# Optimization experiments

Measured on AMD Instinct MI355X. Metric: run time of the kernel, lower is better.

The kernel has to match this reference:

```python
import jax, jax.numpy as jnp
import numpy as np

B, N, D = 16, 4096, 512   # batch, channels, d_model
R, K = 64, 128            # regions, channels per region


def setup_inputs() -> dict:
    key = jax.random.key(0)
    k1, k2, k3 = jax.random.split(key, 3)
    x = jax.random.normal(k1, (B, N, D), dtype=jnp.float32)
    region_indices = jax.random.randint(k2, (R, K), 0, N)
    W = jax.random.normal(k3, (1, D), dtype=jnp.float32) * (1.0 / np.sqrt(D))
    b = jnp.zeros((1,), dtype=jnp.float32)
    return {"x": x, "region_indices": region_indices, "W": W, "b": b}


def reference(x, region_indices, W, b):
    # Gather all regions at once: [B, R, K, D]
    xr = x[:, region_indices, :]
    # Tiny linear scorer 512 -> 1: [B, R, K]
    score = jnp.einsum('brkd,d->brk', xr, W[0]) + b[0]
    # Softmax over the K channels of each region
    attn = jax.nn.softmax(score, axis=-1)
    # Attention-weighted sum over region channels: [B, R, D]
    return jnp.einsum('brk,brkd->brd', attn, xr)
```

## Files before the change

### kernel.cpp

```cpp
#include <hip/hip_runtime.h>
#include <math.h>

constexpr int B = 16;
constexpr int N = 4096;
constexpr int D = 512;
constexpr int R = 64;
constexpr int K = 128;
constexpr int WAVES = 8;
constexpr int KPW = K / WAVES;

__global__ __launch_bounds__(512, 8) void regional_attn_fused(
    const float* __restrict__ x,
    const int*   __restrict__ idx,
    const float* __restrict__ W,
    float* __restrict__ out)
{
    const int v    = blockIdx.x;
    const int xcd  = v & 7;
    const int slot = v >> 3;
    const int b    = xcd * 2 + (slot >> 6);
    const int r    = slot & 63;

    const int tid  = threadIdx.x;
    const int lane = tid & 63;
    const int wave = tid >> 6;

    __shared__ int   s_idx[K];
    __shared__ float s_O[WAVES][D];
    __shared__ float s_m[WAVES];
    __shared__ float s_l[WAVES];

    if (tid < K) s_idx[tid] = idx[r * K + tid];

    const float4* W4 = (const float4*)W;
    const float4  w0 = W4[lane];
    const float4  w1 = W4[lane + 64];

    __syncthreads();

    const float* xb = x + (size_t)b * N * D;
    const int kbase = wave * KPW;

    float  m = -INFINITY;
    float  l = 0.0f;
    float4 O0 = make_float4(0.f, 0.f, 0.f, 0.f);
    float4 O1 = make_float4(0.f, 0.f, 0.f, 0.f);

    const float4* row = (const float4*)(xb + (size_t)s_idx[kbase] * D);
    float4 a0 = row[lane];
    float4 a1 = row[lane + 64];

    #pragma unroll 2
    for (int kk = 0; kk < KPW; ++kk) {
        float4 b0 = a0, b1 = a1;
        if (kk + 1 < KPW) {
            const float4* nrow = (const float4*)(xb + (size_t)s_idx[kbase + kk + 1] * D);
            a0 = nrow[lane];
            a1 = nrow[lane + 64];
        }
        float p = b0.x * w0.x + b0.y * w0.y + b0.z * w0.z + b0.w * w0.w
                + b1.x * w1.x + b1.y * w1.y + b1.z * w1.z + b1.w * w1.w;
        #pragma unroll
        for (int off = 1; off < 64; off <<= 1)
            p += __shfl_xor(p, off, 64);
        float m_new  = fmaxf(m, p);
        float alpha  = __expf(m - m_new);
        float e      = __expf(p - m_new);
        m = m_new;
        l = l * alpha + e;
        O0.x = O0.x * alpha + e * b0.x;
        O0.y = O0.y * alpha + e * b0.y;
        O0.z = O0.z * alpha + e * b0.z;
        O0.w = O0.w * alpha + e * b0.w;
        O1.x = O1.x * alpha + e * b1.x;
        O1.y = O1.y * alpha + e * b1.y;
        O1.z = O1.z * alpha + e * b1.z;
        O1.w = O1.w * alpha + e * b1.w;
    }

    ((float4*)&s_O[wave][0])[lane]      = O0;
    ((float4*)&s_O[wave][0])[lane + 64] = O1;
    if (lane == 0) { s_m[wave] = m; s_l[wave] = l; }
    __syncthreads();

    float M = s_m[0];
    #pragma unroll
    for (int w = 1; w < WAVES; ++w) M = fmaxf(M, s_m[w]);
    float ew[WAVES];
    float denom = 0.0f;
    #pragma unroll
    for (int w = 0; w < WAVES; ++w) {
        ew[w] = __expf(s_m[w] - M);
        denom += s_l[w] * ew[w];
    }
    const float inv = 1.0f / denom;

    const int d = tid;
    float o = 0.0f;
    #pragma unroll
    for (int w = 0; w < WAVES; ++w) o += s_O[w][d] * ew[w];

    out[((size_t)b * R + r) * D + d] = o * inv;
}

extern "C" void kernel_launch(void* const* d_in, const int* in_sizes, int n_in,
                              void* d_out, int out_size, void* d_ws, size_t ws_size,
                              hipStream_t stream) {
    const float* x    = (const float*)d_in[0];
    const int*   idx  = (const int*)d_in[1];
    const float* W    = (const float*)d_in[2];
    float* out = (float*)d_out;

    dim3 grid(B * R);
    dim3 block(512);
    regional_attn_fused<<<grid, block, 0, stream>>>(x, idx, W, out);
}
```

Measured before the change: 196.3 us.

## Precompute per-channel scores in a separate pass, then do exact-softmax weighted accumulation

Splits the fused online-softmax kernel into two launches. The first computes the dot-product score once for every (batch, channel) row into a global buffer. The second gathers the 128 precomputed scores per region, runs an exact softmax in one wave, and accumulates weighted rows with deeper prefetch. This removes the serial online-softmax rescaling and the per-row shuffle reductions from the gather loop, and it avoids recomputing scores for channels that appear in several regions. In exchange the first pass streams the whole x tensor (all 4096 channels, not only the gathered ones) and adds a second launch.

```diff
diff --git a/kernel.cpp b/kernel.cpp
--- a/kernel.cpp
+++ b/kernel.cpp
@@ -9,10 +9,46 @@
 constexpr int WAVES = 8;
 constexpr int KPW = K / WAVES;
 
-__global__ __launch_bounds__(512, 8) void regional_attn_fused(
+__device__ float g_scores[B * N];
+
+__global__ __launch_bounds__(256, 8) void score_pass(
+    const float* __restrict__ x,
+    const float* __restrict__ W)
+{
+    const int tid  = threadIdx.x;
+    const int lane = tid & 63;
+    const int wave = tid >> 6;
+
+    const float4* W4 = (const float4*)W;
+    const float4  w0 = W4[lane];
+    const float4  w1 = W4[lane + 64];
+
+    const size_t gw   = (size_t)blockIdx.x * 4 + wave;
+    const size_t row0 = gw * 8;
+    const float4* xr  = (const float4*)(x + row0 * D);
+
+    float4 a0 = xr[lane];
+    float4 a1 = xr[lane + 64];
+
+    #pragma unroll
+    for (int i = 0; i < 8; ++i) {
+        float4 u0 = a0, u1 = a1;
+        if (i + 1 < 8) {
+            a0 = xr[(size_t)(i + 1) * 128 + lane];
+            a1 = xr[(size_t)(i + 1) * 128 + lane + 64];
+        }
+        float p = u0.x * w0.x + u0.y * w0.y + u0.z * w0.z + u0.w * w0.w
+                + u1.x * w1.x + u1.y * w1.y + u1.z * w1.z + u1.w * w1.w;
+        #pragma unroll
+        for (int off = 1; off < 64; off <<= 1)
+            p += __shfl_xor(p, off, 64);
+        if (lane == 0) g_scores[row0 + i] = p;
+    }
+}
+
+__global__ __launch_bounds__(512, 8) void accum_pass(
     const float* __restrict__ x,
     const int*   __restrict__ idx,
-    const float* __restrict__ W,
     float* __restrict__ out)
 {
     const int v    = blockIdx.x;
@@ -26,81 +62,66 @@
     const int wave = tid >> 6;
 
     __shared__ int   s_idx[K];
+    __shared__ float s_sc[K];
+    __shared__ float s_at[K];
     __shared__ float s_O[WAVES][D];
-    __shared__ float s_m[WAVES];
-    __shared__ float s_l[WAVES];
 
     if (tid < K) s_idx[tid] = idx[r * K + tid];
-
-    const float4* W4 = (const float4*)W;
-    const float4  w0 = W4[lane];
-    const float4  w1 = W4[lane + 64];
-
     __syncthreads();
 
-    const float* xb = x + (size_t)b * N * D;
-    const int kbase = wave * KPW;
+    const float* xb  = x + (size_t)b * N * D;
+    const int kbase  = wave * KPW;
+    const float4* rp0 = (const float4*)(xb + (size_t)s_idx[kbase] * D);
+    float4 a0 = rp0[lane], a1 = rp0[lane + 64];
+    const float4* rp1 = (const float4*)(xb + (size_t)s_idx[kbase + 1] * D);
+    float4 c0 = rp1[lane], c1 = rp1[lane + 64];
 
-    float  m = -INFINITY;
-    float  l = 0.0f;
+    if (tid < K) s_sc[tid] = g_scores[b * N + s_idx[tid]];
+    __syncthreads();
+
+    if (wave == 0) {
+        float p0 = s_sc[lane], p1 = s_sc[lane + 64];
+        float m = fmaxf(p0, p1);
+        #pragma unroll
+        for (int off = 1; off < 64; off <<= 1)
+            m = fmaxf(m, __shfl_xor(m, off, 64));
+        float e0 = __expf(p0 - m);
+        float e1 = __expf(p1 - m);
+        float s = e0 + e1;
+        #pragma unroll
+        for (int off = 1; off < 64; off <<= 1)
+            s += __shfl_xor(s, off, 64);
+        const float inv = 1.0f / s;
+        s_at[lane]      = e0 * inv;
+        s_at[lane + 64] = e1 * inv;
+    }
+    __syncthreads();
+
     float4 O0 = make_float4(0.f, 0.f, 0.f, 0.f);
     float4 O1 = make_float4(0.f, 0.f, 0.f, 0.f);
 
-    const float4* row = (const float4*)(xb + (size_t)s_idx[kbase] * D);
-    float4 a0 = row[lane];
-    float4 a1 = row[lane + 64];
-
-    #pragma unroll 2
+    #pragma unroll
     for (int kk = 0; kk < KPW; ++kk) {
-        float4 b0 = a0, b1 = a1;
-        if (kk + 1 < KPW) {
-            const float4* nrow = (const float4*)(xb + (size_t)s_idx[kbase + kk + 1] * D);
-            a0 = nrow[lane];
-            a1 = nrow[lane + 64];
+        const float wt = s_at[kbase + kk];
+        float4 u0 = a0, u1 = a1;
+        a0 = c0; a1 = c1;
+        if (kk + 2 < KPW) {
+            const float4* rn = (const float4*)(xb + (size_t)s_idx[kbase + kk + 2] * D);
+            c0 = rn[lane]; c1 = rn[lane + 64];
         }
-        float p = b0.x * w0.x + b0.y * w0.y + b0.z * w0.z + b0.w * w0.w
-                + b1.x * w1.x + b1.y * w1.y + b1.z * w1.z + b1.w * w1.w;
-        #pragma unroll
-        for (int off = 1; off < 64; off <<= 1)
-            p += __shfl_xor(p, off, 64);
-        float m_new  = fmaxf(m, p);
-        float alpha  = __expf(m - m_new);
-        float e      = __expf(p - m_new);
-        m = m_new;
-        l = l * alpha + e;
-        O0.x = O0.x * alpha + e * b0.x;
-        O0.y = O0.y * alpha + e * b0.y;
-        O0.z = O0.z * alpha + e * b0.z;
-        O0.w = O0.w * alpha + e * b0.w;
-        O1.x = O1.x * alpha + e * b1.x;
-        O1.y = O1.y * alpha + e * b1.y;
-        O1.z = O1.z * alpha + e * b1.z;
-        O1.w = O1.w * alpha + e * b1.w;
+        O0.x += wt * u0.x; O0.y += wt * u0.y; O0.z += wt * u0.z; O0.w += wt * u0.w;
+        O1.x += wt * u1.x; O1.y += wt * u1.y; O1.z += wt * u1.z; O1.w += wt * u1.w;
     }
 
     ((float4*)&s_O[wave][0])[lane]      = O0;
     ((float4*)&s_O[wave][0])[lane + 64] = O1;
-    if (lane == 0) { s_m[wave] = m; s_l[wave] = l; }
     __syncthreads();
-
-    float M = s_m[0];
-    #pragma unroll
-    for (int w = 1; w < WAVES; ++w) M = fmaxf(M, s_m[w]);
-    float ew[WAVES];
-    float denom = 0.0f;
-    #pragma unroll
-    for (int w = 0; w < WAVES; ++w) {
-        ew[w] = __expf(s_m[w] - M);
-        denom += s_l[w] * ew[w];
-    }
-    const float inv = 1.0f / denom;
 
     const int d = tid;
     float o = 0.0f;
     #pragma unroll
-    for (int w = 0; w < WAVES; ++w) o += s_O[w][d] * ew[w];
-
-    out[((size_t)b * R + r) * D + d] = o * inv;
+    for (int w = 0; w < WAVES; ++w) o += s_O[w][d];
+    out[((size_t)b * R + r) * D + d] = o;
 }
 
 extern "C" void kernel_launch(void* const* d_in, const int* in_sizes, int n_in,
@@ -111,7 +132,6 @@
     const float* W    = (const float*)d_in[2];
     float* out = (float*)d_out;
 
-    dim3 grid(B * R);
-    dim3 block(512);
-    regional_attn_fused<<<grid, block, 0, stream>>>(x, idx, W, out);
+    score_pass<<<dim3(2048), dim3(256), 0, stream>>>(x, W);
+    accum_pass<<<dim3(B * R), dim3(512), 0, stream>>>(x, idx, out);
 }
```

New measurement: 221.6 us. 12.8% more time.

## Stream each unique channel once via inverted index and LDS atomic scatter

Applied to the files above, without the earlier changes.

Builds an inverted index from channel to the regions that contain it. Each batch is then processed in channel chunks, so every referenced row of x is read once instead of once per region occurrence. exp(score)·x is scattered into per-block LDS accumulators with workgroup atomics, and a combine kernel sums the chunk partials and normalizes. This cuts redundant global reads, at the cost of extra launches, LDS atomic contention, partial-buffer traffic, a fixed 16-slot cap on regions per channel, and dropping the max-subtraction that keeps softmax numerically stable.

```diff
diff --git a/kernel.cpp b/kernel.cpp
--- a/kernel.cpp
+++ b/kernel.cpp
@@ -6,112 +6,168 @@
 constexpr int D = 512;
 constexpr int R = 64;
 constexpr int K = 128;
-constexpr int WAVES = 8;
-constexpr int KPW = K / WAVES;
+constexpr int C  = 16;
+constexpr int NC = N / C;
+constexpr int SLOTS = 16;
 
-__global__ __launch_bounds__(512, 8) void regional_attn_fused(
+constexpr size_t OFF_CNT   = 0;
+constexpr size_t OFF_ENTS  = 64  * 1024;
+constexpr size_t OFF_LPART = 512 * 1024;
+constexpr size_t OFF_PART  = 1024 * 1024;
+
+__global__ __launch_bounds__(256) void zero_cnt(int* __restrict__ cnt) {
+    int t = blockIdx.x * 256 + threadIdx.x;
+    if (t < N) cnt[t] = 0;
+}
+
+__global__ __launch_bounds__(256) void build_inv(const int* __restrict__ idx,
+                                                 int* __restrict__ cnt,
+                                                 int* __restrict__ ents) {
+    int e = blockIdx.x * 256 + threadIdx.x;
+    if (e < R * K) {
+        int n = idx[e];
+        int s = atomicAdd(&cnt[n], 1);
+        if (s < SLOTS) ents[n * SLOTS + s] = e >> 7;
+    }
+}
+
+__global__ __launch_bounds__(1024, 4) void stream_accum(
     const float* __restrict__ x,
-    const int*   __restrict__ idx,
     const float* __restrict__ W,
-    float* __restrict__ out)
+    const int*   __restrict__ cnt,
+    const int*   __restrict__ ents,
+    float* __restrict__ part,
+    float* __restrict__ lpart)
 {
-    const int v    = blockIdx.x;
-    const int xcd  = v & 7;
-    const int slot = v >> 3;
-    const int b    = xcd * 2 + (slot >> 6);
-    const int r    = slot & 63;
+    extern __shared__ float smem[];
+    float* s_acc = smem;
+    float* s_l   = smem + R * D;
+
+    const int b  = blockIdx.x >> 4;
+    const int ch = blockIdx.x & 15;
+    const int n0 = ch * NC;
 
     const int tid  = threadIdx.x;
     const int lane = tid & 63;
     const int wave = tid >> 6;
 
-    __shared__ int   s_idx[K];
-    __shared__ float s_O[WAVES][D];
-    __shared__ float s_m[WAVES];
-    __shared__ float s_l[WAVES];
-
-    if (tid < K) s_idx[tid] = idx[r * K + tid];
+    for (int i = tid; i < R * D + R; i += 1024) smem[i] = 0.0f;
 
     const float4* W4 = (const float4*)W;
-    const float4  w0 = W4[lane];
-    const float4  w1 = W4[lane + 64];
+    const float4 w0 = W4[lane];
+    const float4 w1 = W4[lane + 64];
 
     __syncthreads();
 
     const float* xb = x + (size_t)b * N * D;
-    const int kbase = wave * KPW;
 
-    float  m = -INFINITY;
-    float  l = 0.0f;
-    float4 O0 = make_float4(0.f, 0.f, 0.f, 0.f);
-    float4 O1 = make_float4(0.f, 0.f, 0.f, 0.f);
+    int myc = 0;
+    if (lane < 16) myc = cnt[n0 + wave + 16 * lane];
+    unsigned long long m = __ballot(lane < 16 && myc > 0);
 
-    const float4* row = (const float4*)(xb + (size_t)s_idx[kbase] * D);
-    float4 a0 = row[lane];
-    float4 a1 = row[lane + 64];
-
-    #pragma unroll 2
-    for (int kk = 0; kk < KPW; ++kk) {
-        float4 b0 = a0, b1 = a1;
-        if (kk + 1 < KPW) {
-            const float4* nrow = (const float4*)(xb + (size_t)s_idx[kbase + kk + 1] * D);
-            a0 = nrow[lane];
-            a1 = nrow[lane + 64];
-        }
-        float p = b0.x * w0.x + b0.y * w0.y + b0.z * w0.z + b0.w * w0.w
-                + b1.x * w1.x + b1.y * w1.y + b1.z * w1.z + b1.w * w1.w;
-        #pragma unroll
-        for (int off = 1; off < 64; off <<= 1)
-            p += __shfl_xor(p, off, 64);
-        float m_new  = fmaxf(m, p);
-        float alpha  = __expf(m - m_new);
-        float e      = __expf(p - m_new);
-        m = m_new;
-        l = l * alpha + e;
-        O0.x = O0.x * alpha + e * b0.x;
-        O0.y = O0.y * alpha + e * b0.y;
-        O0.z = O0.z * alpha + e * b0.z;
-        O0.w = O0.w * alpha + e * b0.w;
-        O1.x = O1.x * alpha + e * b1.x;
-        O1.y = O1.y * alpha + e * b1.y;
-        O1.z = O1.z * alpha + e * b1.z;
-        O1.w = O1.w * alpha + e * b1.w;
+    int iA = -1, iB = -1;
+    float4 a0 = make_float4(0.f,0.f,0.f,0.f), a1 = a0, c0v = a0, c1v = a0;
+    if (m) {
+        iA = (int)__builtin_ctzll(m); m &= m - 1;
+        const float4* rp = (const float4*)(xb + (size_t)(n0 + wave + 16 * iA) * D);
+        a0 = rp[lane]; a1 = rp[lane + 64];
+    }
+    if (m) {
+        iB = (int)__builtin_ctzll(m); m &= m - 1;
+        const float4* rp = (const float4*)(xb + (size_t)(n0 + wave + 16 * iB) * D);
+        c0v = rp[lane]; c1v = rp[lane + 64];
     }
 
-    ((float4*)&s_O[wave][0])[lane]      = O0;
-    ((float4*)&s_O[wave][0])[lane + 64] = O1;
-    if (lane == 0) { s_m[wave] = m; s_l[wave] = l; }
+    while (iA >= 0) {
+        const int nA = n0 + wave + 16 * iA;
+        const int cA = __shfl(myc, iA, 64);
+        float4 u0 = a0, u1 = a1;
+        iA = iB; a0 = c0v; a1 = c1v;
+        if (m) {
+            iB = (int)__builtin_ctzll(m); m &= m - 1;
+            const float4* rp = (const float4*)(xb + (size_t)(n0 + wave + 16 * iB) * D);
+            c0v = rp[lane]; c1v = rp[lane + 64];
+        } else iB = -1;
+
+        float p = u0.x*w0.x + u0.y*w0.y + u0.z*w0.z + u0.w*w0.w
+                + u1.x*w1.x + u1.y*w1.y + u1.z*w1.z + u1.w*w1.w;
+        #pragma unroll
+        for (int off = 1; off < 64; off <<= 1) p += __shfl_xor(p, off, 64);
+        const float e = __expf(p);
+
+        const int base = nA * SLOTS;
+        for (int j = 0; j < cA; ++j) {
+            const int r = ents[base + j];
+            float* acc = s_acc + (r << 9);
+            __hip_atomic_fetch_add(acc + lane,        e * u0.x, __ATOMIC_RELAXED, __HIP_MEMORY_SCOPE_WORKGROUP);
+            __hip_atomic_fetch_add(acc + 128 + lane,  e * u0.y, __ATOMIC_RELAXED, __HIP_MEMORY_SCOPE_WORKGROUP);
+            __hip_atomic_fetch_add(acc + 256 + lane,  e * u0.z, __ATOMIC_RELAXED, __HIP_MEMORY_SCOPE_WORKGROUP);
+            __hip_atomic_fetch_add(acc + 384 + lane,  e * u0.w, __ATOMIC_RELAXED, __HIP_MEMORY_SCOPE_WORKGROUP);
+            __hip_atomic_fetch_add(acc + 64 + lane,   e * u1.x, __ATOMIC_RELAXED, __HIP_MEMORY_SCOPE_WORKGROUP);
+            __hip_atomic_fetch_add(acc + 192 + lane,  e * u1.y, __ATOMIC_RELAXED, __HIP_MEMORY_SCOPE_WORKGROUP);
+            __hip_atomic_fetch_add(acc + 320 + lane,  e * u1.z, __ATOMIC_RELAXED, __HIP_MEMORY_SCOPE_WORKGROUP);
+            __hip_atomic_fetch_add(acc + 448 + lane,  e * u1.w, __ATOMIC_RELAXED, __HIP_MEMORY_SCOPE_WORKGROUP);
+            if (lane == 0)
+                __hip_atomic_fetch_add(s_l + r, e, __ATOMIC_RELAXED, __HIP_MEMORY_SCOPE_WORKGROUP);
+        }
+    }
+
     __syncthreads();
 
-    float M = s_m[0];
+    float* pbase = part + (size_t)(b * C + ch) * R * D;
+    for (int i = tid; i < R * D; i += 1024) {
+        const int r = i >> 9, d = i & 511;
+        pbase[i] = s_acc[(r << 9) + ((d & 3) << 7) + (d >> 2)];
+    }
+    if (tid < R) lpart[(b * C + ch) * R + tid] = s_l[tid];
+}
+
+__global__ __launch_bounds__(512, 8) void combine(
+    const float* __restrict__ part,
+    const float* __restrict__ lpart,
+    float* __restrict__ out)
+{
+    const int br = blockIdx.x;
+    const int b  = br >> 6;
+    const int r  = br & 63;
+    const int d  = threadIdx.x;
+
+    float lsum = 0.0f;
     #pragma unroll
-    for (int w = 1; w < WAVES; ++w) M = fmaxf(M, s_m[w]);
-    float ew[WAVES];
-    float denom = 0.0f;
+    for (int c = 0; c < C; ++c) lsum += lpart[(b * C + c) * R + r];
+
+    float sum = 0.0f;
     #pragma unroll
-    for (int w = 0; w < WAVES; ++w) {
-        ew[w] = __expf(s_m[w] - M);
-        denom += s_l[w] * ew[w];
-    }
-    const float inv = 1.0f / denom;
+    for (int c = 0; c < C; ++c)
+        sum += part[((size_t)(b * C + c) * R + r) * D + d];
 
-    const int d = tid;
-    float o = 0.0f;
-    #pragma unroll
-    for (int w = 0; w < WAVES; ++w) o += s_O[w][d] * ew[w];
-
-    out[((size_t)b * R + r) * D + d] = o * inv;
+    out[(size_t)br * D + d] = sum / lsum;
 }
 
 extern "C" void kernel_launch(void* const* d_in, const int* in_sizes, int n_in,
                               void* d_out, int out_size, void* d_ws, size_t ws_size,
                               hipStream_t stream) {
-    const float* x    = (const float*)d_in[0];
-    const int*   idx  = (const int*)d_in[1];
-    const float* W    = (const float*)d_in[2];
+    const float* x   = (const float*)d_in[0];
+    const int*   idx = (const int*)d_in[1];
+    const float* W   = (const float*)d_in[2];
     float* out = (float*)d_out;
 
-    dim3 grid(B * R);
-    dim3 block(512);
-    regional_attn_fused<<<grid, block, 0, stream>>>(x, idx, W, out);
+    char* ws = (char*)d_ws;
+    int*   cnt   = (int*)  (ws + OFF_CNT);
+    int*   ents  = (int*)  (ws + OFF_ENTS);
+    float* lpart = (float*)(ws + OFF_LPART);
+    float* part  = (float*)(ws + OFF_PART);
+
+    constexpr int LDS_BYTES = (R * D + R) * 4;
+    static bool attr_set = false;
+    if (!attr_set) {
+        hipFuncSetAttribute(reinterpret_cast<const void*>(stream_accum),
+                            hipFuncAttributeMaxDynamicSharedMemorySize, LDS_BYTES);
+        attr_set = true;
+    }
+
+    zero_cnt   <<<16,   256, 0,        stream>>>(cnt);
+    build_inv  <<<32,   256, 0,        stream>>>(idx, cnt, ents);
+    stream_accum<<<B*C, 1024, LDS_BYTES, stream>>>(x, W, cnt, ents, part, lpart);
+    combine    <<<B*R,  512, 0,        stream>>>(part, lpart, out);
 }
```

Result: slower. 523.4 us (+166.6%).
